# Performance work log

Hardware: AMD Instinct MI355X
Metric: run time of the kernel (lower is better)

Reference implementation:

```python
import jax, jax.numpy as jnp
import numpy as np

IN_DIM = 512
OUT_DIM = 256


def setup_inputs() -> dict:
    key = jax.random.key(0)
    ks = jax.random.split(key, 5)
    b, n, d, o = 32, 64, IN_DIM, OUT_DIM
    lim1 = 1.0 / np.sqrt(2 * d)
    lim2 = 1.0 / np.sqrt(o)
    return {
        "x": jax.random.normal(ks[0], (b, n, d), dtype=jnp.float32),
        "W1": jax.random.uniform(ks[1], (o, 2 * d), jnp.float32, -lim1, lim1),
        "b1": jax.random.uniform(ks[2], (o,), jnp.float32, -lim1, lim1),
        "W2": jax.random.uniform(ks[3], (o, o), jnp.float32, -lim2, lim2),
        "b2": jax.random.uniform(ks[4], (o,), jnp.float32, -lim2, lim2),
    }


def reference(x, W1, b1, W2, b2):
    # x: [b, n, d]; fc1 over cat(xi, xj) == xi @ Wa.T + xj @ Wb.T + b1
    b, n, d = x.shape
    Wa, Wb = W1[:, :d], W1[:, d:]
    hi = jnp.einsum("bnd,od->bno", x, Wa)  # [b, n, o]
    hj = jnp.einsum("bnd,od->bno", x, Wb)  # [b, n, o]
    h = hi[:, :, None, :] + hj[:, None, :, :] + b1  # [b, n, n, o]
    y = jax.nn.relu(jnp.einsum("bijo,po->bijp", h, W2) + b2)  # [b, n, n, o]
    mask = ~jnp.eye(n, dtype=bool)  # zero self-pairs
    y = y * mask[None, :, :, None]
    return y.sum(axis=2)  # [b, n, o]
```

## Files before the change

kernel.cpp:

```cpp
#include <hip/hip_runtime.h>
#include <hip/hip_bf16.h>


typedef unsigned short u16;
typedef __attribute__((ext_vector_type(8))) short short8v;
typedef __attribute__((ext_vector_type(4))) short short4v;
typedef __attribute__((ext_vector_type(4))) float float4v;
typedef __attribute__((ext_vector_type(2))) float float2v;

typedef __attribute__((address_space(1))) const unsigned char* gas_ptr;
typedef __attribute__((address_space(3))) unsigned char* las_ptr;

__device__ __forceinline__ void lds_load16(const void* g, void* l) {
    __builtin_amdgcn_global_load_lds((gas_ptr)g, (las_ptr)l, 16, 0, 0);
}

__device__ __forceinline__ u16 f2bf(float f) {
    unsigned u = __float_as_uint(f);
    return (u16)((u + 0x7fffu + ((u >> 16) & 1u)) >> 16);
}

__device__ __forceinline__ short8v cvt8v(float4v a, float4v b) {
    union { u16 us[8]; short8v v; } o;
    o.us[0] = f2bf(a.x); o.us[1] = f2bf(a.y); o.us[2] = f2bf(a.z); o.us[3] = f2bf(a.w);
    o.us[4] = f2bf(b.x); o.us[5] = f2bf(b.y); o.us[6] = f2bf(b.z); o.us[7] = f2bf(b.w);
    return o.v;
}

__global__ __launch_bounds__(256) void prep_kernel(
    const float* __restrict__ x, const float* __restrict__ W1,
    const float* __restrict__ b1, const float* __restrict__ W2,
    const float* __restrict__ b2,
    u16* __restrict__ Wfb, u16* __restrict__ xb, float* __restrict__ cvec) {
    const int bid = blockIdx.x;
    const int t = threadIdx.x;
    if (bid >= 65) {
        int base = (bid - 65) * 4096 + t * 16;
        const float* s = x + base;
        float4v a0 = *(const float4v*)s,        a1 = *(const float4v*)(s + 4);
        float4v a2 = *(const float4v*)(s + 8),  a3 = *(const float4v*)(s + 12);
        *(short8v*)&xb[base]     = cvt8v(a0, a1);
        *(short8v*)&xb[base + 8] = cvt8v(a2, a3);
        return;
    }
    if (bid == 64) {
        float acc = b2[t];
        const float4v* wrow = (const float4v*)(W2 + t * 256);
#pragma unroll 8
        for (int o4 = 0; o4 < 64; ++o4) {
            float4v wv = wrow[o4];
            float4v bv = *(const float4v*)(b1 + o4 * 4);
            acc += wv.x * bv.x + wv.y * bv.y + wv.z * bv.z + wv.w * bv.w;
        }
        cvec[t] = acc;
        return;
    }

    __shared__ __align__(16) u16 As[64 * 264];
    __shared__ __align__(16) u16 Bt[64 * 264];
    const int qt = bid >> 3, dt = bid & 7;
    const int q0 = qt * 64, d0 = dt * 64;
    const int p0 = q0 & 255;
    const int off = (q0 & 256) * 2;
    const int lane = t & 63, w = t >> 6;
    const int rQ = lane >> 4, rM = lane & 15;

#pragma unroll
    for (int rr = 0; rr < 8; ++rr) {
        int row = w * 16 + rr * 2 + (lane >> 5);
        int c = lane & 31;
        const float* s = W2 + (p0 + row) * 256 + c * 8;
        float4v a0 = *(const float4v*)s, a1 = *(const float4v*)(s + 4);
        *(short8v*)&As[row * 264 + c * 8] = cvt8v(a0, a1);
    }
#pragma unroll
    for (int kk = 0; kk < 4; ++kk) {
        const int m = t & 15, og = t >> 4;
        const int o0 = kk * 64 + og * 4;
        const int d4 = m * 4;
        float4v f0 = *(const float4v*)(W1 + (o0 + 0) * 1024 + off + d0 + d4);
        float4v f1 = *(const float4v*)(W1 + (o0 + 1) * 1024 + off + d0 + d4);
        float4v f2 = *(const float4v*)(W1 + (o0 + 2) * 1024 + off + d0 + d4);
        float4v f3 = *(const float4v*)(W1 + (o0 + 3) * 1024 + off + d0 + d4);
        const int u = o0 >> 3, sub = o0 & 7;
#pragma unroll
        for (int dd = 0; dd < 4; ++dd) {
            int d = d4 + dd;
            int usw = u ^ ((d >> 3) & 7);
            union { u16 us[4]; short4v v; } pk;
            pk.us[0] = f2bf(f0[dd]); pk.us[1] = f2bf(f1[dd]);
            pk.us[2] = f2bf(f2[dd]); pk.us[3] = f2bf(f3[dd]);
            *(short4v*)&Bt[d * 264 + usw * 8 + sub] = pk.v;
        }
    }
    __syncthreads();

    const int wm = w >> 1, wn = w & 1;
    float4v acc[2][2] = {};
#pragma unroll
    for (int ks = 0; ks < 8; ++ks) {
        short8v a[2], bf[2];
#pragma unroll
        for (int mf = 0; mf < 2; ++mf) {
            int row = wm * 32 + mf * 16 + rM;
            a[mf] = *(const short8v*)&As[row * 264 + (ks * 4 + rQ) * 8];
        }
#pragma unroll
        for (int nf = 0; nf < 2; ++nf) {
            int drow = wn * 32 + nf * 16 + rM;
            int ku = (ks * 4 + rQ) ^ ((drow >> 3) & 7);
            bf[nf] = *(const short8v*)&Bt[drow * 264 + ku * 8];
        }
#pragma unroll
        for (int mf = 0; mf < 2; ++mf)
#pragma unroll
            for (int nf = 0; nf < 2; ++nf)
                acc[mf][nf] = __builtin_amdgcn_mfma_f32_16x16x32_bf16(
                    a[mf], bf[nf], acc[mf][nf], 0, 0, 0);
    }

#pragma unroll
    for (int mf = 0; mf < 2; ++mf)
#pragma unroll
        for (int nf = 0; nf < 2; ++nf)
#pragma unroll
            for (int r = 0; r < 4; ++r) {
                int q = q0 + wm * 32 + mf * 16 + rQ * 4 + r;
                int d = d0 + wn * 32 + nf * 16 + rM;
                Wfb[q * 512 + d] = f2bf(acc[mf][nf][r]);
            }
}

__global__ __launch_bounds__(512, 1) void fused_kernel(
    const u16* __restrict__ xb, const u16* __restrict__ Wfb,
    const float* __restrict__ cvec, float* __restrict__ out) {
    __shared__ __align__(16) u16 smem[2 * 64 * 520];
    u16* Xs = smem;
    u16* Ws = smem + 64 * 520;
    const int bid = blockIdx.x;
    const int b = bid & 31, pc = bid >> 5;
    const int p0 = pc * 32;
    const int tid = threadIdx.x;
    const int lane = tid & 63, w = tid >> 6;
    const int rQ = lane >> 4, rM = lane & 15;
    const int uv = w & 1, rh = w >> 1;

#pragma unroll
    for (int rr = 0; rr < 8; ++rr) {
        int row = w * 8 + rr;
        lds_load16(xb + (b * 64 + row) * 512 + lane * 8, (void*)&Xs[row * 520]);
    }
#pragma unroll
    for (int rr = 0; rr < 8; ++rr) {
        int row = w * 8 + rr;
        int q = (row < 32) ? (p0 + row) : (256 + p0 + (row - 32));
        lds_load16(Wfb + q * 512 + lane * 8, (void*)&Ws[row * 520]);
    }
    __syncthreads();

    float4v acc[2] = {};
#pragma unroll
    for (int ks = 0; ks < 16; ++ks) {
        short8v a = *(const short8v*)&Xs[(rh * 16 + rM) * 520 + (ks * 4 + rQ) * 8];
#pragma unroll
        for (int nf = 0; nf < 2; ++nf) {
            int brow = uv * 32 + nf * 16 + rM;
            short8v bf = *(const short8v*)&Ws[brow * 520 + (ks * 4 + rQ) * 8];
            acc[nf] = __builtin_amdgcn_mfma_f32_16x16x32_bf16(a, bf, acc[nf], 0, 0, 0);
        }
    }
    __syncthreads();

    float* Us = (float*)smem;
    float* Vs = Us + 64 * 34;
    float* dst = uv ? Vs : Us;
#pragma unroll
    for (int nf = 0; nf < 2; ++nf)
#pragma unroll
        for (int r = 0; r < 4; ++r)
            dst[(rh * 16 + rQ * 4 + r) * 34 + nf * 16 + rM] = acc[nf][r];
    __syncthreads();

    const int p2 = tid & 15;
    const int ig = tid >> 4;
    float2v cv = *(const float2v*)(cvec + p0 + p2 * 2);
    float2v u2[2], acc2[2];
#pragma unroll
    for (int ii = 0; ii < 2; ++ii) {
        float2v uu = *(const float2v*)&Us[(ig * 2 + ii) * 34 + p2 * 2];
        u2[ii].x = uu.x + cv.x; u2[ii].y = uu.y + cv.y;
        acc2[ii].x = 0.f; acc2[ii].y = 0.f;
    }
#pragma unroll 8
    for (int j = 0; j < 64; ++j) {
        float2v v = *(const float2v*)&Vs[j * 34 + p2 * 2];
#pragma unroll
        for (int ii = 0; ii < 2; ++ii) {
            acc2[ii].x += fmaxf(u2[ii].x + v.x, 0.f);
            acc2[ii].y += fmaxf(u2[ii].y + v.y, 0.f);
        }
    }
#pragma unroll
    for (int ii = 0; ii < 2; ++ii) {
        int i = ig * 2 + ii;
        float2v vd = *(const float2v*)&Vs[i * 34 + p2 * 2];
        acc2[ii].x -= fmaxf(u2[ii].x + vd.x, 0.f);
        acc2[ii].y -= fmaxf(u2[ii].y + vd.y, 0.f);
        *(float2v*)&out[(b * 64 + i) * 256 + p0 + p2 * 2] = acc2[ii];
    }
}

extern "C" void kernel_launch(void* const* d_in, const int* in_sizes, int n_in,
                              void* d_out, int out_size, void* d_ws, size_t ws_size,
                              hipStream_t stream) {
    const float* x  = (const float*)d_in[0];
    const float* W1 = (const float*)d_in[1];
    const float* b1 = (const float*)d_in[2];
    const float* W2 = (const float*)d_in[3];
    const float* b2 = (const float*)d_in[4];
    float* out = (float*)d_out;

    u16* Wfb = (u16*)d_ws;
    u16* xb  = Wfb + 512 * 512;
    float* cvec = (float*)(xb + 2048 * 512);

    prep_kernel<<<321, 256, 0, stream>>>(x, W1, b1, W2, b2, Wfb, xb, cvec);
    fused_kernel<<<256, 512, 0, stream>>>(xb, Wfb, cvec, out);
}
```

Before: 21.18 us.

## Retile prep GEMM to 32x128 tiles, give U/V their own LDS region, drop a barrier

The prep weight-fold GEMM now uses 32-row by 128-column tiles, 64 blocks across q and d, instead of 64x64 tiles. Each thread loads 16 contiguous floats per W1 row, and each wave computes a 16x64 output strip with four MFMAs per A fragment. The fused kernel puts the U/V float staging in a separate LDS region after the X/W tiles, which removes one __syncthreads between the MFMA loop and the staging stores. It also issues the Wfb loads before the xb loads. The cost is more shared memory per block (about 147 KB in the fused kernel) and a different LDS footprint and register use in prep.

```diff
diff --git a/kernel.cpp b/kernel.cpp
--- a/kernel.cpp
+++ b/kernel.cpp
@@ -56,87 +56,84 @@
         return;
     }
 
-    __shared__ __align__(16) u16 As[64 * 264];
-    __shared__ __align__(16) u16 Bt[64 * 264];
-    const int qt = bid >> 3, dt = bid & 7;
-    const int q0 = qt * 64, d0 = dt * 64;
-    const int p0 = q0 & 255;
+    __shared__ __align__(16) u16 As[32 * 264];
+    __shared__ __align__(16) u16 Bt[128 * 264];
+    const int qt = bid >> 2, dt = bid & 3;
+    const int q0 = qt * 32, d0 = dt * 128;
+    const int pw = q0 & 255;
     const int off = (q0 & 256) * 2;
     const int lane = t & 63, w = t >> 6;
     const int rQ = lane >> 4, rM = lane & 15;
 
 #pragma unroll
-    for (int rr = 0; rr < 8; ++rr) {
-        int row = w * 16 + rr * 2 + (lane >> 5);
+    for (int rr = 0; rr < 4; ++rr) {
+        int row = w * 8 + rr * 2 + (lane >> 5);
         int c = lane & 31;
-        const float* s = W2 + (p0 + row) * 256 + c * 8;
+        const float* s = W2 + (pw + row) * 256 + c * 8;
         float4v a0 = *(const float4v*)s, a1 = *(const float4v*)(s + 4);
         *(short8v*)&As[row * 264 + c * 8] = cvt8v(a0, a1);
     }
 #pragma unroll
-    for (int kk = 0; kk < 4; ++kk) {
-        const int m = t & 15, og = t >> 4;
-        const int o0 = kk * 64 + og * 4;
-        const int d4 = m * 4;
-        float4v f0 = *(const float4v*)(W1 + (o0 + 0) * 1024 + off + d0 + d4);
-        float4v f1 = *(const float4v*)(W1 + (o0 + 1) * 1024 + off + d0 + d4);
-        float4v f2 = *(const float4v*)(W1 + (o0 + 2) * 1024 + off + d0 + d4);
-        float4v f3 = *(const float4v*)(W1 + (o0 + 3) * 1024 + off + d0 + d4);
-        const int u = o0 >> 3, sub = o0 & 7;
-#pragma unroll
-        for (int dd = 0; dd < 4; ++dd) {
-            int d = d4 + dd;
-            int usw = u ^ ((d >> 3) & 7);
+    for (int s2 = 0; s2 < 2; ++s2) {
+        const int u = t * 2 + s2;
+        const int o0 = (u & 63) * 4;
+        const int dbase = (u >> 6) * 16;
+        const float* s0 = W1 + o0 * 1024 + off + d0 + dbase;
+        float4v f[4][4];
+#pragma unroll
+        for (int j = 0; j < 4; ++j)
+#pragma unroll
+            for (int q4 = 0; q4 < 4; ++q4)
+                f[j][q4] = *(const float4v*)(s0 + j * 1024 + q4 * 4);
+        const int ubase = o0 >> 3, sub = o0 & 7;
+#pragma unroll
+        for (int dd = 0; dd < 16; ++dd) {
+            int d = dbase + dd;
+            int usw = ubase ^ ((d >> 3) & 7);
             union { u16 us[4]; short4v v; } pk;
-            pk.us[0] = f2bf(f0[dd]); pk.us[1] = f2bf(f1[dd]);
-            pk.us[2] = f2bf(f2[dd]); pk.us[3] = f2bf(f3[dd]);
+            pk.us[0] = f2bf(f[0][dd >> 2][dd & 3]);
+            pk.us[1] = f2bf(f[1][dd >> 2][dd & 3]);
+            pk.us[2] = f2bf(f[2][dd >> 2][dd & 3]);
+            pk.us[3] = f2bf(f[3][dd >> 2][dd & 3]);
             *(short4v*)&Bt[d * 264 + usw * 8 + sub] = pk.v;
         }
     }
     __syncthreads();
 
-    const int wm = w >> 1, wn = w & 1;
-    float4v acc[2][2] = {};
+    const int qh = (w & 1) * 16, dq = (w >> 1) * 64;
+    float4v acc[4] = {};
 #pragma unroll
     for (int ks = 0; ks < 8; ++ks) {
-        short8v a[2], bf[2];
-#pragma unroll
-        for (int mf = 0; mf < 2; ++mf) {
-            int row = wm * 32 + mf * 16 + rM;
-            a[mf] = *(const short8v*)&As[row * 264 + (ks * 4 + rQ) * 8];
-        }
-#pragma unroll
-        for (int nf = 0; nf < 2; ++nf) {
-            int drow = wn * 32 + nf * 16 + rM;
+        short8v a = *(const short8v*)&As[(qh + rM) * 264 + (ks * 4 + rQ) * 8];
+#pragma unroll
+        for (int nf = 0; nf < 4; ++nf) {
+            int drow = dq + nf * 16 + rM;
             int ku = (ks * 4 + rQ) ^ ((drow >> 3) & 7);
-            bf[nf] = *(const short8v*)&Bt[drow * 264 + ku * 8];
-        }
-#pragma unroll
-        for (int mf = 0; mf < 2; ++mf)
-#pragma unroll
-            for (int nf = 0; nf < 2; ++nf)
-                acc[mf][nf] = __builtin_amdgcn_mfma_f32_16x16x32_bf16(
-                    a[mf], bf[nf], acc[mf][nf], 0, 0, 0);
-    }
-
-#pragma unroll
-    for (int mf = 0; mf < 2; ++mf)
-#pragma unroll
-        for (int nf = 0; nf < 2; ++nf)
-#pragma unroll
-            for (int r = 0; r < 4; ++r) {
-                int q = q0 + wm * 32 + mf * 16 + rQ * 4 + r;
-                int d = d0 + wn * 32 + nf * 16 + rM;
-                Wfb[q * 512 + d] = f2bf(acc[mf][nf][r]);
-            }
-}
+            short8v bf = *(const short8v*)&Bt[drow * 264 + ku * 8];
+            acc[nf] = __builtin_amdgcn_mfma_f32_16x16x32_bf16(a, bf, acc[nf], 0, 0, 0);
+        }
+    }
+#pragma unroll
+    for (int nf = 0; nf < 4; ++nf)
+#pragma unroll
+        for (int r = 0; r < 4; ++r) {
+            int q = q0 + qh + rQ * 4 + r;
+            int d = d0 + dq + nf * 16 + rM;
+            Wfb[q * 512 + d] = f2bf(acc[nf][r]);
+        }
+}
+
+#define UV_OFF 133120
+#define FUSED_LDS (133120 + 2 * 64 * 34 * 4)
 
 __global__ __launch_bounds__(512, 1) void fused_kernel(
     const u16* __restrict__ xb, const u16* __restrict__ Wfb,
     const float* __restrict__ cvec, float* __restrict__ out) {
-    __shared__ __align__(16) u16 smem[2 * 64 * 520];
-    u16* Xs = smem;
-    u16* Ws = smem + 64 * 520;
+    __shared__ __align__(16) unsigned char smem[FUSED_LDS];
+    u16* Xs = (u16*)smem;
+    u16* Ws = (u16*)smem + 64 * 520;
+    float* Us = (float*)(smem + UV_OFF);
+    float* Vs = Us + 64 * 34;
     const int bid = blockIdx.x;
     const int b = bid & 31, pc = bid >> 5;
     const int p0 = pc * 32;
@@ -148,13 +145,13 @@
 #pragma unroll
     for (int rr = 0; rr < 8; ++rr) {
         int row = w * 8 + rr;
-        lds_load16(xb + (b * 64 + row) * 512 + lane * 8, (void*)&Xs[row * 520]);
+        int q = (row < 32) ? (p0 + row) : (256 + p0 + (row - 32));
+        lds_load16(Wfb + q * 512 + lane * 8, (void*)&Ws[row * 520]);
     }
 #pragma unroll
     for (int rr = 0; rr < 8; ++rr) {
         int row = w * 8 + rr;
-        int q = (row < 32) ? (p0 + row) : (256 + p0 + (row - 32));
-        lds_load16(Wfb + q * 512 + lane * 8, (void*)&Ws[row * 520]);
+        lds_load16(xb + (b * 64 + row) * 512 + lane * 8, (void*)&Xs[row * 520]);
     }
     __syncthreads();
 
@@ -169,10 +166,7 @@
             acc[nf] = __builtin_amdgcn_mfma_f32_16x16x32_bf16(a, bf, acc[nf], 0, 0, 0);
         }
     }
-    __syncthreads();
-
-    float* Us = (float*)smem;
-    float* Vs = Us + 64 * 34;
+
     float* dst = uv ? Vs : Us;
 #pragma unroll
     for (int nf = 0; nf < 2; ++nf)
```

Result: no change. 21.23 us (+0.3%).
